# Kernel tuning notes

Hardware: AMD Instinct MI355X
Metric: run time of the kernel (lower is better)

## Reference

```python
import jax, jax.numpy as jnp
import numpy as np

H = 8
D_MODEL = 512
D_K = D_MODEL // H
NEG = -1e9


def setup_inputs() -> dict:
    key = jax.random.key(0)
    ks = jax.random.split(key, 11)
    B, S = 2, 2048
    scale = 1.0 / np.sqrt(D_MODEL)
    inp = {
        'query': jax.random.normal(ks[0], (B, S, D_MODEL), dtype=jnp.float32),
        'key': jax.random.normal(ks[1], (B, S, D_MODEL), dtype=jnp.float32),
        'value': jax.random.normal(ks[2], (B, S, D_MODEL), dtype=jnp.float32),
        'Wq': jax.random.normal(ks[3], (D_MODEL, D_MODEL), dtype=jnp.float32) * scale,
        'bq': jnp.zeros((D_MODEL,), dtype=jnp.float32),
        'Wk': jax.random.normal(ks[4], (D_MODEL, D_MODEL), dtype=jnp.float32) * scale,
        'bk': jnp.zeros((D_MODEL,), dtype=jnp.float32),
        'Wv': jax.random.normal(ks[5], (D_MODEL, D_MODEL), dtype=jnp.float32) * scale,
        'bv': jnp.zeros((D_MODEL,), dtype=jnp.float32),
        'Wo': jax.random.normal(ks[6], (D_MODEL, D_MODEL), dtype=jnp.float32) * scale,
        'bo': jnp.zeros((D_MODEL,), dtype=jnp.float32),
    }
    return inp


def reference(query, key, value, Wq, bq, Wk, bk, Wv, bv, Wo, bo):
    B, S, _ = query.shape
    # QKV projections (nn.Linear: x @ W.T + b), split into heads -> [B, H, S, D_K]
    def proj(x, W, b):
        return (x @ W.T + b).reshape(B, S, H, D_K).transpose(0, 2, 1, 3)

    q = proj(query, Wq, bq)
    k = proj(key, Wk, bk)
    v = proj(value, Wv, bv)

    scores = jnp.einsum('bhqd,bhkd->bhqk', q, k) / jnp.sqrt(jnp.float32(D_K))
    # diagonal mask (mask=True): token cannot attend to itself
    diag = jnp.eye(S, dtype=bool)
    scores = jnp.where(diag, NEG, scores)

    p_attn = jax.nn.softmax(scores, axis=-1)  # [B, H, S, S]
    x = jnp.einsum('bhqk,bhkd->bhqd', p_attn, v)
    x = x.transpose(0, 2, 1, 3).reshape(B, S, H * D_K)
    return x @ Wo.T + bo
```

## Files before the change

### kernel.cpp

```cpp
#include <hip/hip_runtime.h>
#include <hip/hip_bf16.h>
#include <math.h>

#define NUM_H 8
#define DK    64
#define DM    512
#define SEQ   2048
#define NB    2
#define MROWS (NB*SEQ)

typedef unsigned short u16;
typedef unsigned int   u32;
typedef __attribute__((ext_vector_type(8))) __bf16 bf16x8;
typedef __attribute__((ext_vector_type(4))) float  f32x4;

__device__ __forceinline__ u16 f2bf(float v) {
    union { float f; u32 i; } x; x.f = v;
    u32 r = (x.i + 0x7FFFu + ((x.i >> 16) & 1u)) >> 16;
    return (u16)r;
}
__device__ __forceinline__ u16 f2h(float v) {
    union { _Float16 h; u16 u; } x; x.h = (_Float16)v; return x.u;
}
__device__ __forceinline__ float h2f(u16 u) {
    union { u16 u; _Float16 h; } x; x.u = u; return (float)x.h;
}
__device__ __forceinline__ bf16x8 ld_bf8(const u16* p) {
    union { uint4 u; bf16x8 v; } t;
    t.u = *(const uint4*)p;
    return t.v;
}
__device__ __forceinline__ uint4 pack8bf(const float* f) {
    uint4 o;
    o.x = (u32)f2bf(f[0]) | ((u32)f2bf(f[1]) << 16);
    o.y = (u32)f2bf(f[2]) | ((u32)f2bf(f[3]) << 16);
    o.z = (u32)f2bf(f[4]) | ((u32)f2bf(f[5]) << 16);
    o.w = (u32)f2bf(f[6]) | ((u32)f2bf(f[7]) << 16);
    return o;
}

__global__ __launch_bounds__(256) void convW(
    const float* __restrict__ Wq, const float* __restrict__ Wk,
    const float* __restrict__ Wv, const float* __restrict__ Wo,
    u16* __restrict__ Wscr)
{
    const int z = blockIdx.y;
    const float* src = (z == 0) ? Wq : (z == 1) ? Wk : (z == 2) ? Wv : Wo;
    u16* dst = Wscr + (size_t)z * 262144;
    int i = (blockIdx.x * 256 + threadIdx.x) * 8;
    float4 a = *(const float4*)(src + i);
    float4 b = *(const float4*)(src + i + 4);
    float f[8] = {a.x, a.y, a.z, a.w, b.x, b.y, b.z, b.w};
    *(uint4*)&dst[i] = pack8bf(f);
}

#define MODE_QK 0
#define MODE_VT 1
#define MODE_FIN 2

template<int MODE, bool INBF>
__device__ __forceinline__ void gemm_core(
    const void* __restrict__ Xv, const u16* __restrict__ Wb,
    const float* __restrict__ bias, void* __restrict__ outv,
    u16* As, u16* Bs, int row0, int col0)
{
    const int tid = threadIdx.x;
    const int lane = tid & 63, w = tid >> 6;
    const int ln15 = lane & 15, quad = lane >> 4;
    const int wm = (w >> 1) * 32, wn = (w & 1) * 32;

    f32x4 acc[2][2];
#pragma unroll
    for (int mt = 0; mt < 2; ++mt)
#pragma unroll
        for (int nt = 0; nt < 2; ++nt) acc[mt][nt] = (f32x4){0.f, 0.f, 0.f, 0.f};

    for (int kt = 0; kt < DM; kt += 64) {
        __syncthreads();
#pragma unroll
        for (int g = 0; g < 2; ++g) {
            int idx = g * 2048 + tid * 8;
            int r = idx >> 6, c = idx & 63;
            if (INBF) {
                *(uint4*)&As[r * 72 + c] =
                    *(const uint4*)((const u16*)Xv + (size_t)(row0 + r) * DM + kt + c);
            } else {
                const float* xp = (const float*)Xv + (size_t)(row0 + r) * DM + kt + c;
                float4 a = *(const float4*)xp;
                float4 b2 = *(const float4*)(xp + 4);
                float f[8] = {a.x, a.y, a.z, a.w, b2.x, b2.y, b2.z, b2.w};
                *(uint4*)&As[r * 72 + c] = pack8bf(f);
            }
        }
#pragma unroll
        for (int g = 0; g < 2; ++g) {
            int idx = g * 2048 + tid * 8;
            int r = idx >> 6, c = idx & 63;
            *(uint4*)&Bs[r * 72 + c] =
                *(const uint4*)(Wb + (size_t)(col0 + r) * DM + kt + c);
        }
        __syncthreads();

#pragma unroll
        for (int ks = 0; ks < 2; ++ks) {
            bf16x8 af[2], bfr[2];
#pragma unroll
            for (int mt = 0; mt < 2; ++mt)
                af[mt] = ld_bf8(&As[(wm + mt * 16 + ln15) * 72 + ks * 32 + quad * 8]);
#pragma unroll
            for (int nt = 0; nt < 2; ++nt)
                bfr[nt] = ld_bf8(&Bs[(wn + nt * 16 + ln15) * 72 + ks * 32 + quad * 8]);
#pragma unroll
            for (int mt = 0; mt < 2; ++mt)
#pragma unroll
                for (int nt = 0; nt < 2; ++nt)
                    acc[mt][nt] = __builtin_amdgcn_mfma_f32_16x16x32_bf16(
                        af[mt], bfr[nt], acc[mt][nt], 0, 0, 0);
        }
    }

    float bc[2];
#pragma unroll
    for (int nt = 0; nt < 2; ++nt) bc[nt] = bias[col0 + wn + nt * 16 + ln15];
    const int h = col0 >> 6;

    if (MODE == MODE_FIN) {
        float* outF = (float*)outv;
#pragma unroll
        for (int mt = 0; mt < 2; ++mt)
#pragma unroll
            for (int r = 0; r < 4; ++r) {
                int m = row0 + wm + mt * 16 + quad * 4 + r;
#pragma unroll
                for (int nt = 0; nt < 2; ++nt)
                    outF[(size_t)m * DM + col0 + wn + nt * 16 + ln15] = acc[mt][nt][r] + bc[nt];
            }
    } else if (MODE == MODE_QK) {
        u16* outB = (u16*)outv;
#pragma unroll
        for (int mt = 0; mt < 2; ++mt)
#pragma unroll
            for (int r = 0; r < 4; ++r) {
                int m = row0 + wm + mt * 16 + quad * 4 + r;
                int b = m >> 11, s2 = m & (SEQ - 1);
#pragma unroll
                for (int nt = 0; nt < 2; ++nt) {
                    int dk = wn + nt * 16 + ln15;
                    outB[((size_t)((b * NUM_H + h) * SEQ + s2)) * DK + dk] =
                        f2bf(acc[mt][nt][r] + bc[nt]);
                }
            }
    } else {
        u16* outB = (u16*)outv;
        __syncthreads();
#pragma unroll
        for (int mt = 0; mt < 2; ++mt)
#pragma unroll
            for (int nt = 0; nt < 2; ++nt) {
                int dk = wn + nt * 16 + ln15;
#pragma unroll
                for (int r = 0; r < 4; ++r) {
                    int sl = wm + mt * 16 + quad * 4 + r;
                    As[dk * 72 + sl] = f2bf(acc[mt][nt][r] + bc[nt]);
                }
            }
        __syncthreads();
        int dk = tid >> 2, ch = (tid & 3) * 16;
        int b = row0 >> 11, s0 = row0 & (SEQ - 1);
        size_t base = ((size_t)((b * NUM_H + h) * DK + dk)) * SEQ + s0 + ch;
        *(uint4*)&outB[base]     = *(const uint4*)&As[dk * 72 + ch];
        *(uint4*)&outB[base + 8] = *(const uint4*)&As[dk * 72 + ch + 8];
    }
}

__global__ __launch_bounds__(256) void qkv_mfma(
    const float* __restrict__ xq, const float* __restrict__ xk, const float* __restrict__ xv,
    const u16* __restrict__ Wscr,
    const float* __restrict__ b0, const float* __restrict__ b1, const float* __restrict__ b2,
    u16* __restrict__ oQ, u16* __restrict__ oK, u16* __restrict__ oVt)
{
    __shared__ u16 As[64 * 72];
    __shared__ u16 Bs[64 * 72];
    const int row0 = blockIdx.x * 64, col0 = blockIdx.y * 64;
    const int z = blockIdx.z;
    const u16* W = Wscr + (size_t)z * 262144;
    if (z == 2)
        gemm_core<MODE_VT, false>(xv, W, b2, oVt, As, Bs, row0, col0);
    else if (z == 0)
        gemm_core<MODE_QK, false>(xq, W, b0, oQ, As, Bs, row0, col0);
    else
        gemm_core<MODE_QK, false>(xk, W, b1, oK, As, Bs, row0, col0);
}

__global__ __launch_bounds__(256) void final_mfma(
    const u16* __restrict__ X, const u16* __restrict__ Wbf,
    const float* __restrict__ bias, float* __restrict__ out)
{
    __shared__ u16 As[64 * 72];
    __shared__ u16 Bs[64 * 72];
    gemm_core<MODE_FIN, true>(X, Wbf, bias, out, As, Bs,
                              blockIdx.x * 64, blockIdx.y * 64);
}

#define LSTR 72
__global__ __launch_bounds__(256) void attn_mfma(
    const u16* __restrict__ Qg, const u16* __restrict__ Kg,
    const u16* __restrict__ Vtg, u16* __restrict__ Pd, float* __restrict__ Cl)
{
    __shared__ u16 Klds[64 * LSTR];
    __shared__ u16 Vtlds[64 * LSTR];
    __shared__ u16 Pls[64 * LSTR];

    const int tid = threadIdx.x;
    const int lane = tid & 63;
    const int w = tid >> 6;
    const int ln15 = lane & 15;
    const int quad = lane >> 4;
    const int bh = blockIdx.y;
    const int b = bh >> 3, h = bh & 7;
    const int qb = blockIdx.x * 64;
    const int z = blockIdx.z;
    const int k0 = z * (SEQ / 2), k1 = k0 + SEQ / 2;

    const u16* Qp = Qg + (size_t)bh * SEQ * DK;
    const u16* Kp = Kg + (size_t)bh * SEQ * DK;
    const u16* Vp = Vtg + (size_t)bh * DK * SEQ;

    const int qrowA = qb + w * 16 + ln15;
    const bf16x8 qa0 = ld_bf8(&Qp[(size_t)qrowA * DK + quad * 8]);
    const bf16x8 qa1 = ld_bf8(&Qp[(size_t)qrowA * DK + 32 + quad * 8]);

    f32x4 O[4];
    float l_i[4] = {0.f, 0.f, 0.f, 0.f};
#pragma unroll
    for (int nt = 0; nt < 4; ++nt) O[nt] = (f32x4){0.f, 0.f, 0.f, 0.f};

    const int sr = tid >> 3;
    const int scl = (tid & 7) * 8;

    for (int kt = k0; kt < k1; kt += 64) {
        __syncthreads();
        *(uint4*)&Klds[sr * LSTR + scl]         = *(const uint4*)&Kp[(size_t)(kt + sr) * DK + scl];
        *(uint4*)&Klds[(sr + 32) * LSTR + scl]  = *(const uint4*)&Kp[(size_t)(kt + sr + 32) * DK + scl];
        *(uint4*)&Vtlds[sr * LSTR + scl]        = *(const uint4*)&Vp[(size_t)sr * SEQ + kt + scl];
        *(uint4*)&Vtlds[(sr + 32) * LSTR + scl] = *(const uint4*)&Vp[(size_t)(sr + 32) * SEQ + kt + scl];
        __syncthreads();

        const bool diagt = (kt == qb);
#pragma unroll
        for (int nt2 = 0; nt2 < 4; ++nt2) {
            bf16x8 kb0 = ld_bf8(&Klds[(nt2 * 16 + ln15) * LSTR + quad * 8]);
            bf16x8 kb1 = ld_bf8(&Klds[(nt2 * 16 + ln15) * LSTR + 32 + quad * 8]);
            f32x4 zacc = (f32x4){0.f, 0.f, 0.f, 0.f};
            zacc = __builtin_amdgcn_mfma_f32_16x16x32_bf16(qa0, kb0, zacc, 0, 0, 0);
            zacc = __builtin_amdgcn_mfma_f32_16x16x32_bf16(qa1, kb1, zacc, 0, 0, 0);
#pragma unroll
            for (int r = 0; r < 4; ++r) {
                float e = __expf(fmaf(zacc[r], 0.125f, -4.0f));
                if (diagt && (nt2 * 16 + ln15 == w * 16 + quad * 4 + r)) e = 0.f;
                l_i[r] += e;
                Pls[(w * 16 + quad * 4 + r) * LSTR + nt2 * 16 + ln15] = f2bf(e);
            }
        }

        bf16x8 pa0 = ld_bf8(&Pls[(w * 16 + ln15) * LSTR + quad * 8]);
        bf16x8 pa1 = ld_bf8(&Pls[(w * 16 + ln15) * LSTR + 32 + quad * 8]);
#pragma unroll
        for (int nt = 0; nt < 4; ++nt) {
            bf16x8 vb0 = ld_bf8(&Vtlds[(nt * 16 + ln15) * LSTR + quad * 8]);
            bf16x8 vb1 = ld_bf8(&Vtlds[(nt * 16 + ln15) * LSTR + 32 + quad * 8]);
            O[nt] = __builtin_amdgcn_mfma_f32_16x16x32_bf16(pa0, vb0, O[nt], 0, 0, 0);
            O[nt] = __builtin_amdgcn_mfma_f32_16x16x32_bf16(pa1, vb1, O[nt], 0, 0, 0);
        }
    }

#pragma unroll
    for (int r = 0; r < 4; ++r) {
        float s = l_i[r];
        s += __shfl_xor(s, 1);
        s += __shfl_xor(s, 2);
        s += __shfl_xor(s, 4);
        s += __shfl_xor(s, 8);
        l_i[r] = s;
    }
    if (ln15 == 0) {
#pragma unroll
        for (int r = 0; r < 4; ++r)
            Cl[(size_t)z * 32768 + bh * SEQ + qb + w * 16 + quad * 4 + r] = l_i[r];
    }
#pragma unroll
    for (int r = 0; r < 4; ++r) {
        int s = qb + w * 16 + quad * 4 + r;
        size_t base = (size_t)z * 2097152 + ((size_t)(b * SEQ + s)) * DM + h * DK;
#pragma unroll
        for (int nt = 0; nt < 4; ++nt)
            Pd[base + nt * 16 + ln15] = f2h(O[nt][r] * 0.015625f);
    }
}

__global__ __launch_bounds__(256) void combine(
    const u16* __restrict__ Pd, const float* __restrict__ Cl, u16* __restrict__ C)
{
    int idx = (blockIdx.x * 256 + threadIdx.x) * 8;
    int row = idx >> 9, col = idx & 511;
    int b = row >> 11, s = row & (SEQ - 1), h = col >> 6;
    int bh = b * NUM_H + h;
    float lsum = Cl[bh * SEQ + s] + Cl[32768 + bh * SEQ + s];
    float sc = 64.f / lsum;
    uint4 u0 = *(const uint4*)&Pd[idx];
    uint4 u1 = *(const uint4*)&Pd[2097152 + idx];
    u32 a0[4] = {u0.x, u0.y, u0.z, u0.w};
    u32 a1[4] = {u1.x, u1.y, u1.z, u1.w};
    float f[8];
#pragma unroll
    for (int j = 0; j < 4; ++j) {
        f[2 * j]     = (h2f((u16)(a0[j] & 0xffff)) + h2f((u16)(a1[j] & 0xffff))) * sc;
        f[2 * j + 1] = (h2f((u16)(a0[j] >> 16))    + h2f((u16)(a1[j] >> 16)))    * sc;
    }
    *(uint4*)&C[idx] = pack8bf(f);
}

extern "C" void kernel_launch(void* const* d_in, const int* in_sizes, int n_in,
                              void* d_out, int out_size, void* d_ws, size_t ws_size,
                              hipStream_t stream) {
    const float* q  = (const float*)d_in[0];
    const float* k  = (const float*)d_in[1];
    const float* v  = (const float*)d_in[2];
    const float* Wq = (const float*)d_in[3];
    const float* bq = (const float*)d_in[4];
    const float* Wk = (const float*)d_in[5];
    const float* bk = (const float*)d_in[6];
    const float* Wv = (const float*)d_in[7];
    const float* bv = (const float*)d_in[8];
    const float* Wo = (const float*)d_in[9];
    const float* bo = (const float*)d_in[10];
    float* out = (float*)d_out;

    const size_t TSZ = (size_t)MROWS * DM;
    u16* Qb  = (u16*)d_ws;
    u16* Kb  = Qb + TSZ;
    u16* Vtb = Qb + 2 * TSZ;
    u16* CbU = Qb + 3 * TSZ;
    float* Cl  = (float*)CbU;
    u16*  Wscr = CbU + 131072;

    u16* Pd = (u16*)d_out;

    dim3 blk(256);
    hipLaunchKernelGGL(convW, dim3(128, 4), blk, 0, stream, Wq, Wk, Wv, Wo, Wscr);
    dim3 gq(MROWS / 64, DM / 64, 3);
    hipLaunchKernelGGL(qkv_mfma, gq, blk, 0, stream,
                       q, k, v, Wscr, bq, bk, bv, Qb, Kb, Vtb);
    dim3 ga(SEQ / 64, NB * NUM_H, 2);
    hipLaunchKernelGGL(attn_mfma, ga, blk, 0, stream, Qb, Kb, Vtb, Pd, Cl);
    hipLaunchKernelGGL(combine, dim3(1024), blk, 0, stream, Pd, Cl, Qb);
    dim3 gf(MROWS / 64, DM / 64);
    hipLaunchKernelGGL(final_mfma, gf, blk, 0, stream, Qb, Wscr + 3 * 262144, bo, out);
}
```

Baseline: 160.7 us.

## Fuse split-K attention combine into attention kernel and convert weights on the fly

Drops the separate weight-conversion kernel; GEMMs now read fp32 weights and convert them to bf16 while staging into shared memory. Also removes the combine kernel. The two key-halves of each query tile pair up through an atomic counter: the first finisher writes its fp16 partial output and row sums to a slot, and the second spin-waits on a flag, merges, normalizes and writes the bf16 context directly. This saves two launches and one round trip of partial results through memory. In exchange, weight reads are fp32 and repeated across blocks, and the spin-wait can deadlock if the partner block is never scheduled.

```diff
diff --git a/kernel.cpp b/kernel.cpp
--- a/kernel.cpp
+++ b/kernel.cpp
@@ -39,28 +39,13 @@
     return o;
 }
 
-__global__ __launch_bounds__(256) void convW(
-    const float* __restrict__ Wq, const float* __restrict__ Wk,
-    const float* __restrict__ Wv, const float* __restrict__ Wo,
-    u16* __restrict__ Wscr)
-{
-    const int z = blockIdx.y;
-    const float* src = (z == 0) ? Wq : (z == 1) ? Wk : (z == 2) ? Wv : Wo;
-    u16* dst = Wscr + (size_t)z * 262144;
-    int i = (blockIdx.x * 256 + threadIdx.x) * 8;
-    float4 a = *(const float4*)(src + i);
-    float4 b = *(const float4*)(src + i + 4);
-    float f[8] = {a.x, a.y, a.z, a.w, b.x, b.y, b.z, b.w};
-    *(uint4*)&dst[i] = pack8bf(f);
-}
-
 #define MODE_QK 0
 #define MODE_VT 1
 #define MODE_FIN 2
 
 template<int MODE, bool INBF>
 __device__ __forceinline__ void gemm_core(
-    const void* __restrict__ Xv, const u16* __restrict__ Wb,
+    const void* __restrict__ Xv, const float* __restrict__ W,
     const float* __restrict__ bias, void* __restrict__ outv,
     u16* As, u16* Bs, int row0, int col0)
 {
@@ -96,8 +81,11 @@
         for (int g = 0; g < 2; ++g) {
             int idx = g * 2048 + tid * 8;
             int r = idx >> 6, c = idx & 63;
-            *(uint4*)&Bs[r * 72 + c] =
-                *(const uint4*)(Wb + (size_t)(col0 + r) * DM + kt + c);
+            const float* wp = W + (size_t)(col0 + r) * DM + kt + c;
+            float4 a = *(const float4*)wp;
+            float4 b2 = *(const float4*)(wp + 4);
+            float f[8] = {a.x, a.y, a.z, a.w, b2.x, b2.y, b2.z, b2.w};
+            *(uint4*)&Bs[r * 72 + c] = pack8bf(f);
         }
         __syncthreads();
 
@@ -175,15 +163,20 @@
 
 __global__ __launch_bounds__(256) void qkv_mfma(
     const float* __restrict__ xq, const float* __restrict__ xk, const float* __restrict__ xv,
-    const u16* __restrict__ Wscr,
+    const float* __restrict__ Wq, const float* __restrict__ Wk, const float* __restrict__ Wv,
     const float* __restrict__ b0, const float* __restrict__ b1, const float* __restrict__ b2,
-    u16* __restrict__ oQ, u16* __restrict__ oK, u16* __restrict__ oVt)
+    u16* __restrict__ oQ, u16* __restrict__ oK, u16* __restrict__ oVt,
+    u32* __restrict__ zeroReg)
 {
     __shared__ u16 As[64 * 72];
     __shared__ u16 Bs[64 * 72];
+    if (blockIdx.x == 0 && blockIdx.y == 0 && blockIdx.z == 0) {
+#pragma unroll
+        for (int j = 0; j < 4; ++j) zeroReg[j * 256 + threadIdx.x] = 0u;
+    }
     const int row0 = blockIdx.x * 64, col0 = blockIdx.y * 64;
     const int z = blockIdx.z;
-    const u16* W = Wscr + (size_t)z * 262144;
+    const float* W = (z == 0) ? Wq : (z == 1) ? Wk : Wv;
     if (z == 2)
         gemm_core<MODE_VT, false>(xv, W, b2, oVt, As, Bs, row0, col0);
     else if (z == 0)
@@ -193,19 +186,20 @@
 }
 
 __global__ __launch_bounds__(256) void final_mfma(
-    const u16* __restrict__ X, const u16* __restrict__ Wbf,
+    const u16* __restrict__ X, const float* __restrict__ W,
     const float* __restrict__ bias, float* __restrict__ out)
 {
     __shared__ u16 As[64 * 72];
     __shared__ u16 Bs[64 * 72];
-    gemm_core<MODE_FIN, true>(X, Wbf, bias, out, As, Bs,
+    gemm_core<MODE_FIN, true>(X, W, bias, out, As, Bs,
                               blockIdx.x * 64, blockIdx.y * 64);
 }
 
 #define LSTR 72
 __global__ __launch_bounds__(256) void attn_mfma(
     const u16* __restrict__ Qg, const u16* __restrict__ Kg,
-    const u16* __restrict__ Vtg, u16* __restrict__ Pd, float* __restrict__ Cl)
+    const u16* __restrict__ Vtg, u16* __restrict__ Slt, float* __restrict__ Cl,
+    u32* __restrict__ cnt, u16* __restrict__ Cc)
 {
     __shared__ u16 Klds[64 * LSTR];
     __shared__ u16 Vtlds[64 * LSTR];
@@ -283,41 +277,55 @@
         s += __shfl_xor(s, 8);
         l_i[r] = s;
     }
-    if (ln15 == 0) {
-#pragma unroll
-        for (int r = 0; r < 4; ++r)
-            Cl[(size_t)z * 32768 + bh * SEQ + qb + w * 16 + quad * 4 + r] = l_i[r];
-    }
-#pragma unroll
-    for (int r = 0; r < 4; ++r) {
-        int s = qb + w * 16 + quad * 4 + r;
-        size_t base = (size_t)z * 2097152 + ((size_t)(b * SEQ + s)) * DM + h * DK;
-#pragma unroll
-        for (int nt = 0; nt < 4; ++nt)
-            Pd[base + nt * 16 + ln15] = f2h(O[nt][r] * 0.015625f);
-    }
-}
-
-__global__ __launch_bounds__(256) void combine(
-    const u16* __restrict__ Pd, const float* __restrict__ Cl, u16* __restrict__ C)
-{
-    int idx = (blockIdx.x * 256 + threadIdx.x) * 8;
-    int row = idx >> 9, col = idx & 511;
-    int b = row >> 11, s = row & (SEQ - 1), h = col >> 6;
-    int bh = b * NUM_H + h;
-    float lsum = Cl[bh * SEQ + s] + Cl[32768 + bh * SEQ + s];
-    float sc = 64.f / lsum;
-    uint4 u0 = *(const uint4*)&Pd[idx];
-    uint4 u1 = *(const uint4*)&Pd[2097152 + idx];
-    u32 a0[4] = {u0.x, u0.y, u0.z, u0.w};
-    u32 a1[4] = {u1.x, u1.y, u1.z, u1.w};
-    float f[8];
-#pragma unroll
-    for (int j = 0; j < 4; ++j) {
-        f[2 * j]     = (h2f((u16)(a0[j] & 0xffff)) + h2f((u16)(a1[j] & 0xffff))) * sc;
-        f[2 * j + 1] = (h2f((u16)(a0[j] >> 16))    + h2f((u16)(a1[j] >> 16)))    * sc;
-    }
-    *(uint4*)&C[idx] = pack8bf(f);
+
+    const int pair = bh * 32 + blockIdx.x;
+    u32* sig = cnt + 512;
+    u16* slot = Slt + (size_t)pair * 4096;
+    __shared__ int role;
+    if (tid == 0) role = (int)atomicAdd(&cnt[pair], 1u);
+    __syncthreads();
+
+    if (role == 0) {
+#pragma unroll
+        for (int nt = 0; nt < 4; ++nt) {
+            u32 lo = (u32)f2h(O[nt][0] * 0.015625f) | ((u32)f2h(O[nt][1] * 0.015625f) << 16);
+            u32 hi = (u32)f2h(O[nt][2] * 0.015625f) | ((u32)f2h(O[nt][3] * 0.015625f) << 16);
+            *(uint2*)&slot[tid * 16 + nt * 4] = make_uint2(lo, hi);
+        }
+        if (ln15 == 0) {
+#pragma unroll
+            for (int r = 0; r < 4; ++r)
+                Cl[pair * 64 + w * 16 + quad * 4 + r] = l_i[r];
+        }
+        __threadfence();
+        __syncthreads();
+        if (tid == 0) atomicAdd(&sig[pair], 1u);
+    } else {
+        if (tid == 0) {
+            while (atomicAdd(&sig[pair], 0u) == 0u) __builtin_amdgcn_s_sleep(8);
+        }
+        __syncthreads();
+        __threadfence();
+        float oth[4][4];
+#pragma unroll
+        for (int nt = 0; nt < 4; ++nt) {
+            uint2 v = *(const uint2*)&slot[tid * 16 + nt * 4];
+            oth[nt][0] = h2f((u16)(v.x & 0xffff));
+            oth[nt][1] = h2f((u16)(v.x >> 16));
+            oth[nt][2] = h2f((u16)(v.y & 0xffff));
+            oth[nt][3] = h2f((u16)(v.y >> 16));
+        }
+#pragma unroll
+        for (int r = 0; r < 4; ++r) {
+            float lo2 = Cl[pair * 64 + w * 16 + quad * 4 + r];
+            float inv = 1.f / (l_i[r] + lo2);
+            int s = qb + w * 16 + quad * 4 + r;
+            size_t base = ((size_t)(b * SEQ + s)) * DM + h * DK;
+#pragma unroll
+            for (int nt = 0; nt < 4; ++nt)
+                Cc[base + nt * 16 + ln15] = f2bf((O[nt][r] + 64.f * oth[nt][r]) * inv);
+        }
+    }
 }
 
 extern "C" void kernel_launch(void* const* d_in, const int* in_sizes, int n_in,
@@ -340,20 +348,18 @@
     u16* Qb  = (u16*)d_ws;
     u16* Kb  = Qb + TSZ;
     u16* Vtb = Qb + 2 * TSZ;
-    u16* CbU = Qb + 3 * TSZ;
-    float* Cl  = (float*)CbU;
-    u16*  Wscr = CbU + 131072;
-
-    u16* Pd = (u16*)d_out;
+    u16* Cc  = Qb + 3 * TSZ;
+
+    u16*   Slt = (u16*)d_out;
+    float* Cl  = (float*)(Slt + 2097152);
+    u32*   cnt = (u32*)(Cl + 32768);
 
     dim3 blk(256);
-    hipLaunchKernelGGL(convW, dim3(128, 4), blk, 0, stream, Wq, Wk, Wv, Wo, Wscr);
     dim3 gq(MROWS / 64, DM / 64, 3);
     hipLaunchKernelGGL(qkv_mfma, gq, blk, 0, stream,
-                       q, k, v, Wscr, bq, bk, bv, Qb, Kb, Vtb);
+                       q, k, v, Wq, Wk, Wv, bq, bk, bv, Qb, Kb, Vtb, cnt);
     dim3 ga(SEQ / 64, NB * NUM_H, 2);
-    hipLaunchKernelGGL(attn_mfma, ga, blk, 0, stream, Qb, Kb, Vtb, Pd, Cl);
-    hipLaunchKernelGGL(combine, dim3(1024), blk, 0, stream, Pd, Cl, Qb);
+    hipLaunchKernelGGL(attn_mfma, ga, blk, 0, stream, Qb, Kb, Vtb, Slt, Cl, cnt, Cc);
     dim3 gf(MROWS / 64, DM / 64);
-    hipLaunchKernelGGL(final_mfma, gf, blk, 0, stream, Qb, Wscr + 3 * 262144, bo, out);
-}
+    hipLaunchKernelGGL(final_mfma, gf, blk, 0, stream, Cc, Wo, bo, out);
+}
```

After: 265.2 us. 65.1% more time.
